# Kernel optimization log

Hardware: AMD Instinct MI355X
Metric: run time of the kernel (lower is better)

The kernel has to match this reference:

```python
import jax, jax.numpy as jnp
import numpy as np

EPS = 1e-8

def setup_inputs() -> dict:
    key = jax.random.key(0)
    k1, k2, k3, k4 = jax.random.split(key, 4)
    B, S, D = 64, 512, 512
    emb1 = jax.random.normal(k1, (B, S, D), dtype=jnp.float32)
    emb2 = jax.random.normal(k2, (B, S, D), dtype=jnp.float32)
    # contiguous prefix attention masks (first n tokens valid), as assumed by the original
    len1 = jax.random.randint(k3, (B,), S // 4, S + 1)
    len2 = jax.random.randint(k4, (B,), S // 4, S + 1)
    pos = jnp.arange(S)
    mask1 = (pos[None, :] < len1[:, None]).astype(jnp.int32)
    mask2 = (pos[None, :] < len2[:, None]).astype(jnp.int32)
    return {"article_1_emb": emb1, "article_2_emb": emb2,
            "article_1_att_mask": mask1, "article_2_att_mask": mask2}


def reference(article_1_emb, article_2_emb, article_1_att_mask, article_2_att_mask):
    # L2-normalize token embeddings (cosine similarity = dot of normalized vectors)
    def l2n(x):
        n = jnp.sqrt(jnp.sum(x * x, axis=-1, keepdims=True))
        return x / jnp.maximum(n, EPS)

    e1 = l2n(article_1_emb)   # [B, S1, D]
    e2 = l2n(article_2_emb)   # [B, S2, D]
    sim = jnp.einsum('bid,bjd->bij', e1, e2)  # [B, S1, S2] pairwise cosine sims

    m1 = article_1_att_mask.astype(jnp.bool_)  # [B, S1]
    m2 = article_2_att_mask.astype(jnp.bool_)  # [B, S2]
    NEG = jnp.float32(-1e9)

    # max over valid j for each valid i, and max over valid i for each valid j
    row_max = jnp.max(jnp.where(m2[:, None, :], sim, NEG), axis=2)  # [B, S1]
    col_max = jnp.max(jnp.where(m1[:, :, None], sim, NEG), axis=1)  # [B, S2]
    row_sum = jnp.sum(jnp.where(m1, row_max, 0.0), axis=1)          # [B]
    col_sum = jnp.sum(jnp.where(m2, col_max, 0.0), axis=1)          # [B]

    n1 = jnp.sum(article_1_att_mask, axis=1).astype(jnp.float32)
    n2 = jnp.sum(article_2_att_mask, axis=1).astype(jnp.float32)
    return (row_sum + col_sum) / (n1 + n2)
```

## Files before the change

kernel.cpp:

```cpp
#include <hip/hip_runtime.h>
#include <hip/hip_bf16.h>


typedef __attribute__((ext_vector_type(8))) short bf16x8;
typedef __attribute__((ext_vector_type(4))) float f32x4;

#define NEGBIG (-1e9f)

__device__ __forceinline__ unsigned packbf2_hw(float lo, float hi) {
    __hip_bfloat162 h = __float22bfloat162_rn(float2{lo, hi});
    union { __hip_bfloat162 h; unsigned u; } c; c.h = h;
    return c.u;
}

__global__ __launch_bounds__(256)
void sim_fused(const float* __restrict__ e1, const float* __restrict__ e2,
               const int* __restrict__ m1g, const int* __restrict__ m2g,
               float* __restrict__ rowmax_p,
               float* __restrict__ colmax_p)
{
    const int rt  = blockIdx.x;
    const int ct  = blockIdx.y;
    const int b   = blockIdx.z;
    const int tid = threadIdx.x;
    const int lane = tid & 63;
    const int w    = tid >> 6;
    const int wm   = w >> 1;
    const int wn   = w & 1;
    const int q    = lane >> 4;
    const int ln   = lane & 15;
    const int nb   = ct * 128;

    __shared__ __align__(16) ushort sA[2][128 * 32];
    __shared__ __align__(16) ushort sB[2][128 * 32];
    __shared__ float spr[2][128];
    __shared__ float spc[2][128];
    __shared__ int   sm1[128], sm2[128];
    __shared__ float sinv1[128], sinv2[128];

    if (tid < 128) sm1[tid] = m1g[b * 512 + rt * 128 + tid];
    else           sm2[tid - 128] = m2g[b * 512 + nb + (tid - 128)];

    const int r = tid >> 1;
    const int h = tid & 1;
    const int s = (r ^ (r >> 2)) & 3;
    const float* gA = e1 + ((size_t)(b * 512 + rt * 128 + r)) * 512 + h * 16;
    const float* gB = e2 + ((size_t)(b * 512 + nb + r)) * 512 + h * 16;
    const int wo0 = r * 32 + (((2 * h)     ^ s) << 3);
    const int wo1 = r * 32 + (((2 * h + 1) ^ s) << 3);

    const int sln = (ln & 3) ^ ((ln >> 2) & 3);
    int aoff[4], boff[4];
    #pragma unroll
    for (int mt = 0; mt < 4; ++mt)
        aoff[mt] = (wm * 64 + mt * 16 + ln) * 32 + ((q ^ sln) << 3);
    #pragma unroll
    for (int nt = 0; nt < 4; ++nt)
        boff[nt] = (wn * 64 + nt * 16 + ln) * 32 + ((q ^ sln) << 3);

    float ssA = 0.f, ssB = 0.f;
    float4 ra[4], rb[4];

    auto LOADK = [&](int kf) {
        const float4* pa = reinterpret_cast<const float4*>(gA + kf);
        const float4* pb = reinterpret_cast<const float4*>(gB + kf);
        ra[0] = pa[0]; ra[1] = pa[1]; ra[2] = pa[2]; ra[3] = pa[3];
        rb[0] = pb[0]; rb[1] = pb[1]; rb[2] = pb[2]; rb[3] = pb[3];
    };
    auto CVTWRITE = [&](int p) {
        #pragma unroll
        for (int i = 0; i < 4; ++i) {
            ssA += ra[i].x * ra[i].x + ra[i].y * ra[i].y
                 + ra[i].z * ra[i].z + ra[i].w * ra[i].w;
            ssB += rb[i].x * rb[i].x + rb[i].y * rb[i].y
                 + rb[i].z * rb[i].z + rb[i].w * rb[i].w;
        }
        uint4 u;
        u.x = packbf2_hw(ra[0].x, ra[0].y); u.y = packbf2_hw(ra[0].z, ra[0].w);
        u.z = packbf2_hw(ra[1].x, ra[1].y); u.w = packbf2_hw(ra[1].z, ra[1].w);
        *reinterpret_cast<uint4*>(&sA[p][wo0]) = u;
        u.x = packbf2_hw(ra[2].x, ra[2].y); u.y = packbf2_hw(ra[2].z, ra[2].w);
        u.z = packbf2_hw(ra[3].x, ra[3].y); u.w = packbf2_hw(ra[3].z, ra[3].w);
        *reinterpret_cast<uint4*>(&sA[p][wo1]) = u;
        u.x = packbf2_hw(rb[0].x, rb[0].y); u.y = packbf2_hw(rb[0].z, rb[0].w);
        u.z = packbf2_hw(rb[1].x, rb[1].y); u.w = packbf2_hw(rb[1].z, rb[1].w);
        *reinterpret_cast<uint4*>(&sB[p][wo0]) = u;
        u.x = packbf2_hw(rb[2].x, rb[2].y); u.y = packbf2_hw(rb[2].z, rb[2].w);
        u.z = packbf2_hw(rb[3].x, rb[3].y); u.w = packbf2_hw(rb[3].z, rb[3].w);
        *reinterpret_cast<uint4*>(&sB[p][wo1]) = u;
    };

    f32x4 acc[4][4];
    #pragma unroll
    for (int i = 0; i < 4; ++i)
        #pragma unroll
        for (int j = 0; j < 4; ++j)
            acc[i][j] = (f32x4){0.f, 0.f, 0.f, 0.f};

    LOADK(0);
    CVTWRITE(0);
    LOADK(32);
    __syncthreads();

    #pragma unroll 2
    for (int k = 0; k < 16; ++k) {
        const int p = k & 1;
        bf16x8 af[4], bfr[4];
        #pragma unroll
        for (int mt = 0; mt < 4; ++mt)
            af[mt] = *reinterpret_cast<const bf16x8*>(&sA[p][aoff[mt]]);
        #pragma unroll
        for (int nt = 0; nt < 4; ++nt)
            bfr[nt] = *reinterpret_cast<const bf16x8*>(&sB[p][boff[nt]]);
        if (k < 15) CVTWRITE(p ^ 1);
        if (k < 14) LOADK((k + 2) * 32);
        #pragma unroll
        for (int mt = 0; mt < 4; ++mt)
            #pragma unroll
            for (int nt = 0; nt < 4; ++nt)
                acc[mt][nt] = __builtin_amdgcn_mfma_f32_16x16x32_bf16(
                    af[mt], bfr[nt], acc[mt][nt], 0, 0, 0);
        __syncthreads();
    }

    ssA += __shfl_xor(ssA, 1);
    ssB += __shfl_xor(ssB, 1);
    if (h == 0) {
        sinv1[r] = 1.0f / fmaxf(sqrtf(ssA), 1e-8f);
        sinv2[r] = 1.0f / fmaxf(sqrtf(ssB), 1e-8f);
    }
    __syncthreads();

    float invj[4];
    f32x4 invi[4];
    #pragma unroll
    for (int nt = 0; nt < 4; ++nt)
        invj[nt] = sinv2[wn * 64 + nt * 16 + ln];
    #pragma unroll
    for (int mt = 0; mt < 4; ++mt)
        #pragma unroll
        for (int rg = 0; rg < 4; ++rg)
            invi[mt][rg] = sinv1[wm * 64 + mt * 16 + q * 4 + rg];
    #pragma unroll
    for (int mt = 0; mt < 4; ++mt)
        #pragma unroll
        for (int nt = 0; nt < 4; ++nt)
            acc[mt][nt] = acc[mt][nt] * (invi[mt] * invj[nt]);

    #pragma unroll
    for (int mt = 0; mt < 4; ++mt) {
        #pragma unroll
        for (int rg = 0; rg < 4; ++rg) {
            float rm = NEGBIG;
            #pragma unroll
            for (int nt = 0; nt < 4; ++nt) {
                float v = sm2[wn * 64 + nt * 16 + ln] ? acc[mt][nt][rg] : NEGBIG;
                rm = fmaxf(rm, v);
            }
            rm = fmaxf(rm, __shfl_xor(rm, 1));
            rm = fmaxf(rm, __shfl_xor(rm, 2));
            rm = fmaxf(rm, __shfl_xor(rm, 4));
            rm = fmaxf(rm, __shfl_xor(rm, 8));
            if (ln == 0) spr[wn][wm * 64 + mt * 16 + q * 4 + rg] = rm;
        }
    }
    #pragma unroll
    for (int nt = 0; nt < 4; ++nt) {
        float cm = NEGBIG;
        #pragma unroll
        for (int mt = 0; mt < 4; ++mt)
            #pragma unroll
            for (int rg = 0; rg < 4; ++rg) {
                float v = sm1[wm * 64 + mt * 16 + q * 4 + rg] ? acc[mt][nt][rg] : NEGBIG;
                cm = fmaxf(cm, v);
            }
        cm = fmaxf(cm, __shfl_xor(cm, 16));
        cm = fmaxf(cm, __shfl_xor(cm, 32));
        if (lane < 16) spc[wm][wn * 64 + nt * 16 + ln] = cm;
    }
    __syncthreads();
    if (tid < 128) {
        rowmax_p[((size_t)b * 4 + ct) * 512 + rt * 128 + tid] =
            fmaxf(spr[0][tid], spr[1][tid]);
        colmax_p[((size_t)b * 4 + rt) * 512 + nb + tid] =
            fmaxf(spc[0][tid], spc[1][tid]);
    }
}

__global__ __launch_bounds__(256)
void final_kernel(const int* __restrict__ m1g, const int* __restrict__ m2g,
                  const float* __restrict__ rowmax_p, const float* __restrict__ colmax_p,
                  float* __restrict__ out)
{
    const int b = blockIdx.x;
    const int tid = threadIdx.x;
    const int lane = tid & 63;
    const int w = tid >> 6;

    float sum = 0.f;
    float nn  = 0.f;
    for (int j = tid; j < 512; j += 256) {
        int mm1 = m1g[b * 512 + j];
        int mm2 = m2g[b * 512 + j];
        nn += (float)(mm1 + mm2);
        const float* rp = rowmax_p + (size_t)b * 2048 + j;
        float rm = fmaxf(fmaxf(rp[0], rp[512]), fmaxf(rp[1024], rp[1536]));
        if (mm1) sum += rm;
        const float* cp = colmax_p + (size_t)b * 2048 + j;
        float cm = fmaxf(fmaxf(cp[0], cp[512]), fmaxf(cp[1024], cp[1536]));
        if (mm2) sum += cm;
    }
    #pragma unroll
    for (int m = 32; m; m >>= 1) {
        sum += __shfl_xor(sum, m);
        nn  += __shfl_xor(nn, m);
    }
    __shared__ float ssum[4], snn[4];
    if (lane == 0) { ssum[w] = sum; snn[w] = nn; }
    __syncthreads();
    if (tid == 0) {
        float S = ssum[0] + ssum[1] + ssum[2] + ssum[3];
        float N = snn[0] + snn[1] + snn[2] + snn[3];
        out[b] = S / N;
    }
}

extern "C" void kernel_launch(void* const* d_in, const int* in_sizes, int n_in,
                              void* d_out, int out_size, void* d_ws, size_t ws_size,
                              hipStream_t stream) {
    const float* e1 = (const float*)d_in[0];
    const float* e2 = (const float*)d_in[1];
    const int*   m1 = (const int*)d_in[2];
    const int*   m2 = (const int*)d_in[3];
    float* out = (float*)d_out;

    float* ws = (float*)d_ws;
    float* rowmax_p = ws;
    float* colmax_p = ws + 131072;

    sim_fused<<<dim3(4, 4, 64), 256, 0, stream>>>(e1, e2, m1, m2,
                                                  rowmax_p, colmax_p);
    final_kernel<<<64, 256, 0, stream>>>(m1, m2, rowmax_p, colmax_p, out);
}
```

Measured before the change: 183.8 us.

## Deepen global prefetch, remap blocks for XCD L2 locality, refine LDS swizzle

Changes the grid to a 1D launch with a block-id remap so that the 2x2 tiles sharing the same row/column strips of one batch land on the same XCD, improving L2 reuse of the fp32 inputs. Register prefetch is deepened to two stages so global loads run three k-steps ahead of the MFMA work. The LDS XOR swizzle adds a higher row bit to reduce bank conflicts, and launch bounds request 3 blocks per CU. These add register pressure, which could cause spills or lower occupancy.

```diff
diff --git a/kernel.cpp b/kernel.cpp
--- a/kernel.cpp
+++ b/kernel.cpp
@@ -13,15 +13,23 @@
     return c.u;
 }
 
-__global__ __launch_bounds__(256)
+__global__ __launch_bounds__(256, 3)
 void sim_fused(const float* __restrict__ e1, const float* __restrict__ e2,
                const int* __restrict__ m1g, const int* __restrict__ m2g,
                float* __restrict__ rowmax_p,
                float* __restrict__ colmax_p)
 {
-    const int rt  = blockIdx.x;
-    const int ct  = blockIdx.y;
-    const int b   = blockIdx.z;
+    const int id   = blockIdx.x;
+    const int xcd  = id & 7;
+    const int k2   = id >> 3;
+    const int wi   = k2 & 3;
+    const int rg   = k2 >> 2;
+    const int glob = rg * 8 + xcd;
+    const int b    = glob >> 2;
+    const int rq   = glob & 3;
+    const int rt   = ((rq >> 1) << 1) | (wi & 1);
+    const int ct   = ((rq & 1) << 1) | (wi >> 1);
+
     const int tid = threadIdx.x;
     const int lane = tid & 63;
     const int w    = tid >> 6;
@@ -43,50 +51,55 @@
 
     const int r = tid >> 1;
     const int h = tid & 1;
-    const int s = (r ^ (r >> 2)) & 3;
+    const int s = (r ^ (r >> 2) ^ (r >> 4)) & 3;
     const float* gA = e1 + ((size_t)(b * 512 + rt * 128 + r)) * 512 + h * 16;
     const float* gB = e2 + ((size_t)(b * 512 + nb + r)) * 512 + h * 16;
     const int wo0 = r * 32 + (((2 * h)     ^ s) << 3);
     const int wo1 = r * 32 + (((2 * h + 1) ^ s) << 3);
 
-    const int sln = (ln & 3) ^ ((ln >> 2) & 3);
     int aoff[4], boff[4];
     #pragma unroll
-    for (int mt = 0; mt < 4; ++mt)
-        aoff[mt] = (wm * 64 + mt * 16 + ln) * 32 + ((q ^ sln) << 3);
-    #pragma unroll
-    for (int nt = 0; nt < 4; ++nt)
-        boff[nt] = (wn * 64 + nt * 16 + ln) * 32 + ((q ^ sln) << 3);
+    for (int mt = 0; mt < 4; ++mt) {
+        int fr = wm * 64 + mt * 16 + ln;
+        int fs = (fr ^ (fr >> 2) ^ (fr >> 4)) & 3;
+        aoff[mt] = fr * 32 + ((q ^ fs) << 3);
+    }
+    #pragma unroll
+    for (int nt = 0; nt < 4; ++nt) {
+        int fr = wn * 64 + nt * 16 + ln;
+        int fs = (fr ^ (fr >> 2) ^ (fr >> 4)) & 3;
+        boff[nt] = fr * 32 + ((q ^ fs) << 3);
+    }
 
     float ssA = 0.f, ssB = 0.f;
-    float4 ra[4], rb[4];
-
-    auto LOADK = [&](int kf) {
+    float4 ra[2][4], rb[2][4];
+
+    auto LOADK = [&](int st, int kf) {
         const float4* pa = reinterpret_cast<const float4*>(gA + kf);
         const float4* pb = reinterpret_cast<const float4*>(gB + kf);
-        ra[0] = pa[0]; ra[1] = pa[1]; ra[2] = pa[2]; ra[3] = pa[3];
-        rb[0] = pb[0]; rb[1] = pb[1]; rb[2] = pb[2]; rb[3] = pb[3];
+        ra[st][0] = pa[0]; ra[st][1] = pa[1]; ra[st][2] = pa[2]; ra[st][3] = pa[3];
+        rb[st][0] = pb[0]; rb[st][1] = pb[1]; rb[st][2] = pb[2]; rb[st][3] = pb[3];
     };
-    auto CVTWRITE = [&](int p) {
+    auto CVTWRITE = [&](int p, int st) {
         #pragma unroll
         for (int i = 0; i < 4; ++i) {
-            ssA += ra[i].x * ra[i].x + ra[i].y * ra[i].y
-                 + ra[i].z * ra[i].z + ra[i].w * ra[i].w;
-            ssB += rb[i].x * rb[i].x + rb[i].y * rb[i].y
-                 + rb[i].z * rb[i].z + rb[i].w * rb[i].w;
+            ssA += ra[st][i].x * ra[st][i].x + ra[st][i].y * ra[st][i].y
+                 + ra[st][i].z * ra[st][i].z + ra[st][i].w * ra[st][i].w;
+            ssB += rb[st][i].x * rb[st][i].x + rb[st][i].y * rb[st][i].y
+                 + rb[st][i].z * rb[st][i].z + rb[st][i].w * rb[st][i].w;
         }
         uint4 u;
-        u.x = packbf2_hw(ra[0].x, ra[0].y); u.y = packbf2_hw(ra[0].z, ra[0].w);
-        u.z = packbf2_hw(ra[1].x, ra[1].y); u.w = packbf2_hw(ra[1].z, ra[1].w);
+        u.x = packbf2_hw(ra[st][0].x, ra[st][0].y); u.y = packbf2_hw(ra[st][0].z, ra[st][0].w);
+        u.z = packbf2_hw(ra[st][1].x, ra[st][1].y); u.w = packbf2_hw(ra[st][1].z, ra[st][1].w);
         *reinterpret_cast<uint4*>(&sA[p][wo0]) = u;
-        u.x = packbf2_hw(ra[2].x, ra[2].y); u.y = packbf2_hw(ra[2].z, ra[2].w);
-        u.z = packbf2_hw(ra[3].x, ra[3].y); u.w = packbf2_hw(ra[3].z, ra[3].w);
+        u.x = packbf2_hw(ra[st][2].x, ra[st][2].y); u.y = packbf2_hw(ra[st][2].z, ra[st][2].w);
+        u.z = packbf2_hw(ra[st][3].x, ra[st][3].y); u.w = packbf2_hw(ra[st][3].z, ra[st][3].w);
         *reinterpret_cast<uint4*>(&sA[p][wo1]) = u;
-        u.x = packbf2_hw(rb[0].x, rb[0].y); u.y = packbf2_hw(rb[0].z, rb[0].w);
-        u.z = packbf2_hw(rb[1].x, rb[1].y); u.w = packbf2_hw(rb[1].z, rb[1].w);
+        u.x = packbf2_hw(rb[st][0].x, rb[st][0].y); u.y = packbf2_hw(rb[st][0].z, rb[st][0].w);
+        u.z = packbf2_hw(rb[st][1].x, rb[st][1].y); u.w = packbf2_hw(rb[st][1].z, rb[st][1].w);
         *reinterpret_cast<uint4*>(&sB[p][wo0]) = u;
-        u.x = packbf2_hw(rb[2].x, rb[2].y); u.y = packbf2_hw(rb[2].z, rb[2].w);
-        u.z = packbf2_hw(rb[3].x, rb[3].y); u.w = packbf2_hw(rb[3].z, rb[3].w);
+        u.x = packbf2_hw(rb[st][2].x, rb[st][2].y); u.y = packbf2_hw(rb[st][2].z, rb[st][2].w);
+        u.z = packbf2_hw(rb[st][3].x, rb[st][3].y); u.w = packbf2_hw(rb[st][3].z, rb[st][3].w);
         *reinterpret_cast<uint4*>(&sB[p][wo1]) = u;
     };
 
@@ -97,14 +110,16 @@
         for (int j = 0; j < 4; ++j)
             acc[i][j] = (f32x4){0.f, 0.f, 0.f, 0.f};
 
-    LOADK(0);
-    CVTWRITE(0);
-    LOADK(32);
+    LOADK(1, 0);
+    CVTWRITE(0, 1);
+    LOADK(0, 32);
+    LOADK(1, 64);
     __syncthreads();
 
     #pragma unroll 2
     for (int k = 0; k < 16; ++k) {
-        const int p = k & 1;
+        const int p  = k & 1;
+        const int st = k & 1;
         bf16x8 af[4], bfr[4];
         #pragma unroll
         for (int mt = 0; mt < 4; ++mt)
@@ -112,8 +127,8 @@
         #pragma unroll
         for (int nt = 0; nt < 4; ++nt)
             bfr[nt] = *reinterpret_cast<const bf16x8*>(&sB[p][boff[nt]]);
-        if (k < 15) CVTWRITE(p ^ 1);
-        if (k < 14) LOADK((k + 2) * 32);
+        if (k < 15) CVTWRITE(p ^ 1, st);
+        if (k < 13) LOADK(st, (k + 3) * 32);
         #pragma unroll
         for (int mt = 0; mt < 4; ++mt)
             #pragma unroll
@@ -139,8 +154,8 @@
     #pragma unroll
     for (int mt = 0; mt < 4; ++mt)
         #pragma unroll
-        for (int rg = 0; rg < 4; ++rg)
-            invi[mt][rg] = sinv1[wm * 64 + mt * 16 + q * 4 + rg];
+        for (int rg2 = 0; rg2 < 4; ++rg2)
+            invi[mt][rg2] = sinv1[wm * 64 + mt * 16 + q * 4 + rg2];
     #pragma unroll
     for (int mt = 0; mt < 4; ++mt)
         #pragma unroll
@@ -150,18 +165,18 @@
     #pragma unroll
     for (int mt = 0; mt < 4; ++mt) {
         #pragma unroll
-        for (int rg = 0; rg < 4; ++rg) {
+        for (int rg2 = 0; rg2 < 4; ++rg2) {
             float rm = NEGBIG;
             #pragma unroll
             for (int nt = 0; nt < 4; ++nt) {
-                float v = sm2[wn * 64 + nt * 16 + ln] ? acc[mt][nt][rg] : NEGBIG;
+                float v = sm2[wn * 64 + nt * 16 + ln] ? acc[mt][nt][rg2] : NEGBIG;
                 rm = fmaxf(rm, v);
             }
             rm = fmaxf(rm, __shfl_xor(rm, 1));
             rm = fmaxf(rm, __shfl_xor(rm, 2));
             rm = fmaxf(rm, __shfl_xor(rm, 4));
             rm = fmaxf(rm, __shfl_xor(rm, 8));
-            if (ln == 0) spr[wn][wm * 64 + mt * 16 + q * 4 + rg] = rm;
+            if (ln == 0) spr[wn][wm * 64 + mt * 16 + q * 4 + rg2] = rm;
         }
     }
     #pragma unroll
@@ -170,8 +185,8 @@
         #pragma unroll
         for (int mt = 0; mt < 4; ++mt)
             #pragma unroll
-            for (int rg = 0; rg < 4; ++rg) {
-                float v = sm1[wm * 64 + mt * 16 + q * 4 + rg] ? acc[mt][nt][rg] : NEGBIG;
+            for (int rg2 = 0; rg2 < 4; ++rg2) {
+                float v = sm1[wm * 64 + mt * 16 + q * 4 + rg2] ? acc[mt][nt][rg2] : NEGBIG;
                 cm = fmaxf(cm, v);
             }
         cm = fmaxf(cm, __shfl_xor(cm, 16));
@@ -238,7 +253,6 @@
     float* rowmax_p = ws;
     float* colmax_p = ws + 131072;
 
-    sim_fused<<<dim3(4, 4, 64), 256, 0, stream>>>(e1, e2, m1, m2,
-                                                  rowmax_p, colmax_p);
+    sim_fused<<<1024, 256, 0, stream>>>(e1, e2, m1, m2, rowmax_p, colmax_p);
     final_kernel<<<64, 256, 0, stream>>>(m1, m2, rowmax_p, colmax_p, out);
 }
```

After: 371.1 us. 102% more time.

## Remap block IDs for XCD-local L2 reuse and strengthen LDS swizzle

Applied to the files above, without the earlier changes.

Switches to a 1D grid and remaps block IDs so the four blocks sharing an A or B row-tile of the same batch land on the same XCD (MI355X schedules blocks round-robin across 8 XCDs). Each XCD's private L2 can then serve the repeated fp32 embedding tile reads instead of fetching them again from HBM. The LDS XOR swizzle also folds in r>>4 for both writes and fragment reads, to reduce bank conflicts. Correctness depends on the remap being a bijection over all 1024 blocks and on the write and read swizzles matching.

```diff
diff --git a/kernel.cpp b/kernel.cpp
--- a/kernel.cpp
+++ b/kernel.cpp
@@ -19,9 +19,17 @@
                float* __restrict__ rowmax_p,
                float* __restrict__ colmax_p)
 {
-    const int rt  = blockIdx.x;
-    const int ct  = blockIdx.y;
-    const int b   = blockIdx.z;
+    const int id   = blockIdx.x;
+    const int xcd  = id & 7;
+    const int k2   = id >> 3;
+    const int wi   = k2 & 3;
+    const int rg   = k2 >> 2;
+    const int glob = rg * 8 + xcd;
+    const int b    = glob >> 2;
+    const int rq   = glob & 3;
+    const int rt   = ((rq >> 1) << 1) | (wi & 1);
+    const int ct   = ((rq & 1) << 1) | (wi >> 1);
+
     const int tid = threadIdx.x;
     const int lane = tid & 63;
     const int w    = tid >> 6;
@@ -43,20 +51,25 @@
 
     const int r = tid >> 1;
     const int h = tid & 1;
-    const int s = (r ^ (r >> 2)) & 3;
+    const int s = (r ^ (r >> 2) ^ (r >> 4)) & 3;
     const float* gA = e1 + ((size_t)(b * 512 + rt * 128 + r)) * 512 + h * 16;
     const float* gB = e2 + ((size_t)(b * 512 + nb + r)) * 512 + h * 16;
     const int wo0 = r * 32 + (((2 * h)     ^ s) << 3);
     const int wo1 = r * 32 + (((2 * h + 1) ^ s) << 3);
 
-    const int sln = (ln & 3) ^ ((ln >> 2) & 3);
     int aoff[4], boff[4];
     #pragma unroll
-    for (int mt = 0; mt < 4; ++mt)
-        aoff[mt] = (wm * 64 + mt * 16 + ln) * 32 + ((q ^ sln) << 3);
-    #pragma unroll
-    for (int nt = 0; nt < 4; ++nt)
-        boff[nt] = (wn * 64 + nt * 16 + ln) * 32 + ((q ^ sln) << 3);
+    for (int mt = 0; mt < 4; ++mt) {
+        int fr = wm * 64 + mt * 16 + ln;
+        int fs = (fr ^ (fr >> 2) ^ (fr >> 4)) & 3;
+        aoff[mt] = fr * 32 + ((q ^ fs) << 3);
+    }
+    #pragma unroll
+    for (int nt = 0; nt < 4; ++nt) {
+        int fr = wn * 64 + nt * 16 + ln;
+        int fs = (fr ^ (fr >> 2) ^ (fr >> 4)) & 3;
+        boff[nt] = fr * 32 + ((q ^ fs) << 3);
+    }
 
     float ssA = 0.f, ssB = 0.f;
     float4 ra[4], rb[4];
@@ -139,8 +152,8 @@
     #pragma unroll
     for (int mt = 0; mt < 4; ++mt)
         #pragma unroll
-        for (int rg = 0; rg < 4; ++rg)
-            invi[mt][rg] = sinv1[wm * 64 + mt * 16 + q * 4 + rg];
+        for (int rg2 = 0; rg2 < 4; ++rg2)
+            invi[mt][rg2] = sinv1[wm * 64 + mt * 16 + q * 4 + rg2];
     #pragma unroll
     for (int mt = 0; mt < 4; ++mt)
         #pragma unroll
@@ -150,18 +163,18 @@
     #pragma unroll
     for (int mt = 0; mt < 4; ++mt) {
         #pragma unroll
-        for (int rg = 0; rg < 4; ++rg) {
+        for (int rg2 = 0; rg2 < 4; ++rg2) {
             float rm = NEGBIG;
             #pragma unroll
             for (int nt = 0; nt < 4; ++nt) {
-                float v = sm2[wn * 64 + nt * 16 + ln] ? acc[mt][nt][rg] : NEGBIG;
+                float v = sm2[wn * 64 + nt * 16 + ln] ? acc[mt][nt][rg2] : NEGBIG;
                 rm = fmaxf(rm, v);
             }
             rm = fmaxf(rm, __shfl_xor(rm, 1));
             rm = fmaxf(rm, __shfl_xor(rm, 2));
             rm = fmaxf(rm, __shfl_xor(rm, 4));
             rm = fmaxf(rm, __shfl_xor(rm, 8));
-            if (ln == 0) spr[wn][wm * 64 + mt * 16 + q * 4 + rg] = rm;
+            if (ln == 0) spr[wn][wm * 64 + mt * 16 + q * 4 + rg2] = rm;
         }
     }
     #pragma unroll
@@ -170,8 +183,8 @@
         #pragma unroll
         for (int mt = 0; mt < 4; ++mt)
             #pragma unroll
-            for (int rg = 0; rg < 4; ++rg) {
-                float v = sm1[wm * 64 + mt * 16 + q * 4 + rg] ? acc[mt][nt][rg] : NEGBIG;
+            for (int rg2 = 0; rg2 < 4; ++rg2) {
+                float v = sm1[wm * 64 + mt * 16 + q * 4 + rg2] ? acc[mt][nt][rg2] : NEGBIG;
                 cm = fmaxf(cm, v);
             }
         cm = fmaxf(cm, __shfl_xor(cm, 16));
@@ -238,7 +251,6 @@
     float* rowmax_p = ws;
     float* colmax_p = ws + 131072;
 
-    sim_fused<<<dim3(4, 4, 64), 256, 0, stream>>>(e1, e2, m1, m2,
-                                                  rowmax_p, colmax_p);
+    sim_fused<<<1024, 256, 0, stream>>>(e1, e2, m1, m2, rowmax_p, colmax_p);
     final_kernel<<<64, 256, 0, stream>>>(m1, m2, rowmax_p, colmax_p, out);
 }
```

Result: no change. 184.4 us (+0.3%).
